# Optimization experiments

Hardware: AMD Instinct MI355X
Metric: run time of the kernel (lower is better)

## Reference

```python
import jax, jax.numpy as jnp
import numpy as np
from jax.ops import segment_sum

N_NODES = 50000
N_EDGES = 600000
HIDDEN = 128
N_FEAT = 128
N_CLASSES = 10
N_GRAPHS = 128


def setup_inputs() -> dict:
    key = jax.random.key(0)
    ks = jax.random.split(key, 16)
    x = jax.random.normal(ks[0], (N_NODES, N_FEAT), dtype=jnp.float32)
    edge_index = jax.random.randint(ks[1], (2, N_EDGES), 0, N_NODES, dtype=jnp.int64)
    batch = jnp.sort(jax.random.randint(ks[2], (N_NODES,), 0, N_GRAPHS, dtype=jnp.int64))
    def lin_init(k, fan_in, fan_out):
        s = 1.0 / np.sqrt(fan_in)
        return jax.random.uniform(k, (fan_in, fan_out), jnp.float32, -s, s)
    params = {
        'W1': lin_init(ks[3], N_FEAT, HIDDEN), 'b1': jnp.zeros((HIDDEN,), jnp.float32),
        'W2': lin_init(ks[4], HIDDEN, HIDDEN), 'b2': jnp.zeros((HIDDEN,), jnp.float32),
        'W3': lin_init(ks[5], HIDDEN, HIDDEN), 'b3': jnp.zeros((HIDDEN,), jnp.float32),
        'W4': lin_init(ks[6], HIDDEN, HIDDEN), 'b4': jnp.zeros((HIDDEN,), jnp.float32),
        'W5': lin_init(ks[7], HIDDEN, HIDDEN), 'b5': jnp.zeros((HIDDEN,), jnp.float32),
        'Wfc': lin_init(ks[8], HIDDEN, HIDDEN), 'bfc': jnp.zeros((HIDDEN,), jnp.float32),
        'Wlin': lin_init(ks[9], HIDDEN, N_CLASSES), 'blin': jnp.zeros((N_CLASSES,), jnp.float32),
    }
    return dict(x=x, edge_index=edge_index, batch=batch, **params)


def _gcn_edges(edge_index, n_nodes):
    # PyG GCNConv default: add self-loops, symmetric deg^-1/2 normalization.
    loop = jnp.arange(n_nodes, dtype=edge_index.dtype)
    row = jnp.concatenate([edge_index[0], loop])  # source (messages gathered from)
    col = jnp.concatenate([edge_index[1], loop])  # target (scatter-add into)
    deg = segment_sum(jnp.ones_like(col, dtype=jnp.float32), col, num_segments=n_nodes)
    dinv = jnp.where(deg > 0, jax.lax.rsqrt(deg), 0.0)
    norm = dinv[row] * dinv[col]  # [E+N]
    return row, col, norm


def _gcn_conv(x, W, b, row, col, norm, n_nodes):
    h = x @ W  # [N, out]
    agg = segment_sum(h[row] * norm[:, None], col, num_segments=n_nodes)
    return agg + b


def reference(x, edge_index, batch, W1, b1, W2, b2, W3, b3, W4, b4, W5, b5, Wfc, bfc, Wlin, blin):
    n = x.shape[0]
    row, col, norm = _gcn_edges(edge_index, n)
    h = jax.nn.relu(_gcn_conv(x, W1, b1, row, col, norm, n))
    h = jax.nn.relu(_gcn_conv(h, W2, b2, row, col, norm, n))
    h = jax.nn.relu(_gcn_conv(h, W3, b3, row, col, norm, n))
    h = jax.nn.relu(_gcn_conv(h, W4, b4, row, col, norm, n))
    h = jax.nn.relu(_gcn_conv(h, W5, b5, row, col, norm, n))
    h = jax.nn.relu(h @ Wfc + bfc)
    # global_mean_pool over batch ids
    sums = segment_sum(h, batch, num_segments=N_GRAPHS)
    cnts = segment_sum(jnp.ones((n,), h.dtype), batch, num_segments=N_GRAPHS)
    pooled = sums / jnp.maximum(cnts, 1.0)[:, None]  # [G, H]
    embeddings = pooled
    # dropout p=0.5 is identity in eval mode
    logits = pooled @ Wlin + blin  # [G, C]
    return logits, jnp.squeeze(embeddings)
```

## Files before the change

kernel.cpp:

```cpp
#include <hip/hip_runtime.h>

typedef __attribute__((ext_vector_type(8))) short short8;
typedef __attribute__((ext_vector_type(4))) float floatx4;
typedef __attribute__((ext_vector_type(4))) unsigned uintx4;
typedef __attribute__((ext_vector_type(8))) _Float16 half8;

static __device__ __forceinline__ unsigned short f2bf(float f) {
    unsigned u = __float_as_uint(f);
    u += 0x7fff + ((u >> 16) & 1);
    return (unsigned short)(u >> 16);
}
static __device__ __forceinline__ float bf2f(unsigned short h) {
    return __uint_as_float((unsigned)h << 16);
}
static __device__ __forceinline__ unsigned packsplit(float f) {
    unsigned short hi = f2bf(f);
    unsigned short lo = f2bf(f - bf2f(hi));
    return ((unsigned)hi << 16) | lo;
}


__global__ void count_kernel(const int* __restrict__ ei, int* degi, int E) {
    int e = blockIdx.x * 256 + threadIdx.x;
    if (e < E) atomicAdd(&degi[ei[E + e]], 1);
}

__global__ __launch_bounds__(256) void scan_bsum_kernel(const int* __restrict__ degi,
                                                        float* __restrict__ dinv,
                                                        int* bsum, int n) {
    int tid = threadIdx.x;
    int i = blockIdx.x * 256 + tid;
    int d = (i < n) ? degi[i] : 0;
    if (i < n) dinv[i] = rsqrtf((float)(d + 1));
    int v = d;
    #pragma unroll
    for (int off = 32; off > 0; off >>= 1) v += __shfl_down(v, off);
    __shared__ int ws[4];
    if ((tid & 63) == 0) ws[tid >> 6] = v;
    __syncthreads();
    if (tid == 0) bsum[blockIdx.x] = ws[0] + ws[1] + ws[2] + ws[3];
}

__global__ __launch_bounds__(256) void scan_emit_kernel(const int* __restrict__ degi,
                                                        const int* __restrict__ bsum,
                                                        int* rp, int* cursor, int n, int nb) {
    int tid = threadIdx.x;
    int bid = blockIdx.x;
    int contrib = 0;
    for (int t = tid; t < bid; t += 256) contrib += bsum[t];
    int cr = contrib;
    #pragma unroll
    for (int off = 32; off > 0; off >>= 1) cr += __shfl_down(cr, off);
    __shared__ int wr[4];
    __shared__ int s_boff;
    if ((tid & 63) == 0) wr[tid >> 6] = cr;
    __syncthreads();
    if (tid == 0) s_boff = wr[0] + wr[1] + wr[2] + wr[3];
    __syncthreads();

    int i = bid * 256 + tid;
    int v = (i < n) ? degi[i] : 0;
    int lane = tid & 63, wid = tid >> 6;
    int x = v;
    #pragma unroll
    for (int off = 1; off < 64; off <<= 1) {
        int y = __shfl_up(x, off);
        if (lane >= off) x += y;
    }
    __shared__ int ws[4];
    if (lane == 63) ws[wid] = x;
    __syncthreads();
    if (tid == 0) { int a = 0; for (int j = 0; j < 4; ++j) { int t = ws[j]; ws[j] = a; a += t; } }
    __syncthreads();
    int excl = x - v + ws[wid] + s_boff;
    if (i < n) { rp[i] = excl; cursor[i] = excl; }
    if (i == n - 1) rp[n] = excl + v;
}

__global__ void fill_kernel(const int* __restrict__ ei, const float* __restrict__ dinv,
                            int* cursor, long long* __restrict__ csr, int E) {
    int e = blockIdx.x * 256 + threadIdx.x;
    if (e >= E) return;
    int r = ei[e], c = ei[E + e];
    int pos = atomicAdd(&cursor[c], 1);
    float wv = dinv[r] * dinv[c];
    long long packed = (long long)(unsigned int)r
                     | ((long long)(unsigned int)__float_as_int(wv) << 32);
    csr[pos] = packed;
}


__global__ void packw_kernel(const float* w0, const float* w1, const float* w2,
                             const float* w3, const float* w4, const float* w5,
                             unsigned short* __restrict__ hi, unsigned short* __restrict__ lo) {
    int l = blockIdx.y;
    const float* W = (l == 0) ? w0 : (l == 1) ? w1 : (l == 2) ? w2
                   : (l == 3) ? w3 : (l == 4) ? w4 : w5;
    int idx = blockIdx.x * 256 + threadIdx.x;
    int k = idx >> 7, nn = idx & 127;
    float v = W[k * 128 + nn];
    unsigned short h = f2bf(v);
    unsigned short ls = f2bf(v - bf2f(h));
    hi[l * 16384 + nn * 128 + k] = h;
    lo[l * 16384 + nn * 128 + k] = ls;
}


#define WLDS_STRIDE 260

static __device__ __forceinline__ void stage_w(const unsigned short* __restrict__ Wth,
                                               const unsigned short* __restrict__ Wtl,
                                               unsigned short* Wlds, int tid) {
    #pragma unroll
    for (int it = 0; it < 8; ++it) {
        int c = it * 512 + tid;
        int row = c >> 5, piece = c & 31;
        const unsigned short* src = (piece < 16)
            ? (Wth + (size_t)row * 128 + piece * 8)
            : (Wtl + (size_t)row * 128 + (piece - 16) * 8);
        int dst = row * WLDS_STRIDE + ((piece < 16) ? piece * 8 : 128 + (piece - 16) * 8);
        *(short8*)&Wlds[dst] = *(const short8*)src;
    }
}

static __device__ __forceinline__ void unpack_u(uintx4 u0, uintx4 u1, short8& ah, short8& al) {
    #pragma unroll
    for (int j = 0; j < 4; ++j) {
        ah[j]     = (short)(u0[j] >> 16); al[j]     = (short)(u0[j] & 0xffff);
        ah[4 + j] = (short)(u1[j] >> 16); al[4 + j] = (short)(u1[j] & 0xffff);
    }
}

__global__ __launch_bounds__(512) void gemm_kernel(const unsigned* __restrict__ Ap,
                                                   const unsigned short* __restrict__ Wth,
                                                   const unsigned short* __restrict__ Wtl,
                                                   void* __restrict__ C, int n, int outf) {
    __shared__ unsigned short Wlds[128 * WLDS_STRIDE];
    int tid = threadIdx.x;
    int wave = tid >> 6, lane = tid & 63;
    int m = lane & 15, quad = lane >> 4;
    int row0 = blockIdx.x * 128 + wave * 16;
    int arow = row0 + m; if (arow > n - 1) arow = n - 1;
    size_t n16 = (size_t)n * 16;
    size_t n32 = (size_t)n * 32;
    const unsigned* abase = Ap + (size_t)arow * 16 + (quad & 1) * 8;
    int chalf = quad >> 1;

    uintx4 pa0[4], pa1[4];
    #pragma unroll
    for (int kc = 0; kc < 4; ++kc) {
        const unsigned* ap = abase + (size_t)(2 * kc + chalf) * n16;
        pa0[kc] = *(const uintx4*)ap;
        pa1[kc] = *(const uintx4*)(ap + 4);
    }

    stage_w(Wth, Wtl, Wlds, tid);

    floatx4 acc[8];
    #pragma unroll
    for (int ct = 0; ct < 8; ++ct) acc[ct] = (floatx4){0.f, 0.f, 0.f, 0.f};
    __syncthreads();

    #pragma unroll
    for (int kc = 0; kc < 4; ++kc) {
        short8 ah, al;
        unpack_u(pa0[kc], pa1[kc], ah, al);
        #pragma unroll
        for (int ct = 0; ct < 8; ++ct) {
            int base = (ct * 16 + m) * WLDS_STRIDE + kc * 32 + quad * 8;
            short8 wh = *(const short8*)&Wlds[base];
            short8 wl = *(const short8*)&Wlds[base + 128];
            acc[ct] = __builtin_amdgcn_mfma_f32_16x16x32_bf16(ah, wl, acc[ct], 0, 0, 0);
            acc[ct] = __builtin_amdgcn_mfma_f32_16x16x32_bf16(al, wh, acc[ct], 0, 0, 0);
            acc[ct] = __builtin_amdgcn_mfma_f32_16x16x32_bf16(ah, wh, acc[ct], 0, 0, 0);
        }
    }
    #pragma unroll
    for (int ct = 0; ct < 8; ++ct) {
        #pragma unroll
        for (int r = 0; r < 4; ++r) {
            int row = row0 + quad * 4 + r;
            if (row < n) {
                if (outf) {
                    ((float*)C)[(size_t)row * 128 + ct * 16 + m] = acc[ct][r];
                } else {
                    ((_Float16*)C)[(size_t)(ct >> 1) * n32 + (size_t)row * 32
                                   + (ct & 1) * 16 + m] = (_Float16)acc[ct][r];
                }
            }
        }
    }
}

__global__ __launch_bounds__(512) void gemm0_kernel(const float* __restrict__ X,
                                                    const unsigned short* __restrict__ Wth,
                                                    const unsigned short* __restrict__ Wtl,
                                                    _Float16* __restrict__ C, int n) {
    __shared__ unsigned short Wlds[128 * WLDS_STRIDE];
    int tid = threadIdx.x;
    int wave = tid >> 6, lane = tid & 63;
    int m = lane & 15, quad = lane >> 4;
    int row0 = blockIdx.x * 128 + wave * 16;
    int arow = row0 + m; if (arow > n - 1) arow = n - 1;
    size_t n32 = (size_t)n * 32;
    const float* aptr = X + (size_t)arow * 128 + quad * 8;

    floatx4 pf0[4], pf1[4];
    #pragma unroll
    for (int kc = 0; kc < 4; ++kc) {
        pf0[kc] = *(const floatx4*)(aptr + kc * 32);
        pf1[kc] = *(const floatx4*)(aptr + kc * 32 + 4);
    }

    stage_w(Wth, Wtl, Wlds, tid);

    floatx4 acc[8];
    #pragma unroll
    for (int ct = 0; ct < 8; ++ct) acc[ct] = (floatx4){0.f, 0.f, 0.f, 0.f};
    __syncthreads();

    #pragma unroll
    for (int kc = 0; kc < 4; ++kc) {
        short8 ah, al;
        #pragma unroll
        for (int j = 0; j < 8; ++j) {
            float fv = (j < 4) ? pf0[kc][j] : pf1[kc][j - 4];
            unsigned short h = f2bf(fv);
            ah[j] = (short)h;
            al[j] = (short)f2bf(fv - bf2f(h));
        }
        #pragma unroll
        for (int ct = 0; ct < 8; ++ct) {
            int base = (ct * 16 + m) * WLDS_STRIDE + kc * 32 + quad * 8;
            short8 wh = *(const short8*)&Wlds[base];
            short8 wl = *(const short8*)&Wlds[base + 128];
            acc[ct] = __builtin_amdgcn_mfma_f32_16x16x32_bf16(ah, wl, acc[ct], 0, 0, 0);
            acc[ct] = __builtin_amdgcn_mfma_f32_16x16x32_bf16(al, wh, acc[ct], 0, 0, 0);
            acc[ct] = __builtin_amdgcn_mfma_f32_16x16x32_bf16(ah, wh, acc[ct], 0, 0, 0);
        }
    }
    #pragma unroll
    for (int ct = 0; ct < 8; ++ct) {
        #pragma unroll
        for (int r = 0; r < 4; ++r) {
            int row = row0 + quad * 4 + r;
            if (row < n)
                C[(size_t)(ct >> 1) * n32 + (size_t)row * 32 + (ct & 1) * 16 + m] =
                    (_Float16)acc[ct][r];
        }
    }
}


__global__ __launch_bounds__(256) void agg_kernel(const _Float16* __restrict__ t,
                                                  const float* __restrict__ bias,
                                                  const int* __restrict__ rp,
                                                  const long long* __restrict__ csr,
                                                  const float* __restrict__ dinv,
                                                  unsigned* __restrict__ hp, int n, int nh) {
    int s = blockIdx.x & 7;
    int chunk = s & 3;
    int half = s >> 2;
    int nb = blockIdx.x >> 3;
    int group = threadIdx.x >> 2;
    int lane4 = threadIdx.x & 3;
    int j = half * nh + nb * 64 + group;
    int jend = half ? n : nh;
    if (j >= jend) return;
    size_t n32 = (size_t)n * 32;
    const _Float16* tc = t + (size_t)chunk * n32;
    int c8 = lane4 * 8;
    int p0 = rp[j], p1 = rp[j + 1];

    float dj = dinv[j];
    float wsf = dj * dj;
    half8 vs = *(const half8*)&tc[(size_t)j * 32 + c8];

    float acc[8];
    #pragma unroll
    for (int k = 0; k < 8; ++k) acc[k] = wsf * (float)vs[k];

    for (int p = p0; p < p1; p += 8) {
        int lim = p1 - 1;
        long long e[8];
        #pragma unroll
        for (int i = 0; i < 8; ++i) e[i] = csr[min(p + i, lim)];
        float w[8];
        #pragma unroll
        for (int i = 0; i < 8; ++i)
            w[i] = (p + i < p1) ? __int_as_float((int)(e[i] >> 32)) : 0.f;
        half8 v[8];
        #pragma unroll
        for (int i = 0; i < 8; ++i)
            v[i] = *(const half8*)&tc[(size_t)(int)e[i] * 32 + c8];
        #pragma unroll
        for (int i = 0; i < 8; ++i) {
            #pragma unroll
            for (int k = 0; k < 8; ++k) acc[k] += w[i] * (float)v[i][k];
        }
    }

    int cbase = chunk * 32 + c8;
    float4 b0 = *(const float4*)&bias[cbase];
    float4 b1 = *(const float4*)&bias[cbase + 4];
    float bb[8] = {b0.x, b0.y, b0.z, b0.w, b1.x, b1.y, b1.z, b1.w};
    unsigned st[8];
    #pragma unroll
    for (int k = 0; k < 8; ++k) st[k] = packsplit(fmaxf(acc[k] + bb[k], 0.f));

    size_t n16 = (size_t)n * 16;
    int hc = chunk * 2 + (lane4 >> 1);
    unsigned* dst = &hp[(size_t)hc * n16 + (size_t)j * 16 + (lane4 & 1) * 8];
    *(uint4*)dst = make_uint4(st[0], st[1], st[2], st[3]);
    *(uint4*)(dst + 4) = make_uint4(st[4], st[5], st[6], st[7]);
}


__global__ __launch_bounds__(256) void pool_kernel(const float* __restrict__ t,
                                                   const float* __restrict__ bfc,
                                                   const int* __restrict__ batch,
                                                   const float* __restrict__ Wlin,
                                                   const float* __restrict__ blin,
                                                   float* __restrict__ out, int n) {
    int g = blockIdx.x;
    int tid = threadIdx.x;
    int lo = 0, hi = n;
    while (lo < hi) { int m = (lo + hi) >> 1; if (batch[m] < g) lo = m + 1; else hi = m; }
    int start = lo;
    lo = start; hi = n;
    while (lo < hi) { int m = (lo + hi) >> 1; if (batch[m] < g + 1) lo = m + 1; else hi = m; }
    int end = lo;

    int lane = tid & 31, sub = tid >> 5;
    int c4 = lane * 4;
    float4 bv = *(const float4*)&bfc[c4];
    float sx = 0.f, sy = 0.f, sz = 0.f, sw = 0.f;
    for (int j = start + sub; j < end; j += 8) {
        float4 v = *(const float4*)&t[(size_t)j * 128 + c4];
        sx += fmaxf(v.x + bv.x, 0.f);
        sy += fmaxf(v.y + bv.y, 0.f);
        sz += fmaxf(v.z + bv.z, 0.f);
        sw += fmaxf(v.w + bv.w, 0.f);
    }
    __shared__ float red[8][128];
    red[sub][c4] = sx; red[sub][c4 + 1] = sy; red[sub][c4 + 2] = sz; red[sub][c4 + 3] = sw;
    __syncthreads();
    __shared__ float pooled[128];
    if (tid < 128) {
        float s = 0.f;
        #pragma unroll
        for (int k = 0; k < 8; ++k) s += red[k][tid];
        float pv = s / fmaxf((float)(end - start), 1.f);
        pooled[tid] = pv;
        out[1280 + g * 128 + tid] = pv;
    }
    __syncthreads();
    if (tid < 10) {
        float a = blin[tid];
        for (int k = 0; k < 128; ++k) a += pooled[k] * Wlin[k * 10 + tid];
        out[g * 10 + tid] = a;
    }
}


extern "C" void kernel_launch(void* const* d_in, const int* in_sizes, int n_in,
                              void* d_out, int out_size, void* d_ws, size_t ws_size,
                              hipStream_t stream) {
    const float* x     = (const float*)d_in[0];
    const int*   ei    = (const int*)d_in[1];
    const int*   batch = (const int*)d_in[2];
    const float* Wl[6] = {(const float*)d_in[3], (const float*)d_in[5], (const float*)d_in[7],
                          (const float*)d_in[9], (const float*)d_in[11], (const float*)d_in[13]};
    const float* bl[6] = {(const float*)d_in[4], (const float*)d_in[6], (const float*)d_in[8],
                          (const float*)d_in[10], (const float*)d_in[12], (const float*)d_in[14]};
    const float* Wlin = (const float*)d_in[15];
    const float* blin = (const float*)d_in[16];

    const int N = in_sizes[2];
    const int E = in_sizes[1] / 2;
    (void)n_in; (void)out_size; (void)ws_size;

    char* p = (char*)d_ws;
    auto carve = [&](size_t bytes) { void* r = (void*)p; p += (bytes + 255) & ~(size_t)255; return r; };
    void*           treg   = carve((size_t)N * 128 * 4);
    _Float16*       th     = (_Float16*)treg;
    float*          tf     = (float*)treg;
    unsigned*       hp     = (unsigned*)carve((size_t)N * 128 * 4);
    int*            degi   = (int*)carve((size_t)N * 4);
    float*          dinv   = (float*)carve((size_t)N * 4);
    int*            rp     = (int*)carve((size_t)(N + 1) * 4);
    int*            cursor = (int*)carve((size_t)N * 4);
    long long*      csr    = (long long*)carve((size_t)(E + N) * 8);
    int*            bsum   = (int*)carve(256 * 4);
    unsigned short* wth    = (unsigned short*)carve(6 * 16384 * 2);
    unsigned short* wtl    = (unsigned short*)carve(6 * 16384 * 2);

    int gN = (N + 255) / 256;
    hipMemsetAsync(degi, 0, (size_t)N * 4, stream);
    count_kernel<<<(E + 255) / 256, 256, 0, stream>>>(ei, degi, E);
    scan_bsum_kernel<<<gN, 256, 0, stream>>>(degi, dinv, bsum, N);
    scan_emit_kernel<<<gN, 256, 0, stream>>>(degi, bsum, rp, cursor, N, gN);
    fill_kernel<<<(E + 255) / 256, 256, 0, stream>>>(ei, dinv, cursor, csr, E);
    packw_kernel<<<dim3(64, 6), 256, 0, stream>>>(Wl[0], Wl[1], Wl[2], Wl[3], Wl[4], Wl[5],
                                                  wth, wtl);

    int NH = (N + 1) / 2;
    int gGemm = (N + 127) / 128;
    int gAgg  = 8 * ((NH + 63) / 64);
    gemm0_kernel<<<gGemm, 512, 0, stream>>>(x, wth, wtl, th, N);
    agg_kernel<<<gAgg, 256, 0, stream>>>(th, bl[0], rp, csr, dinv, hp, N, NH);
    for (int l = 1; l < 5; ++l) {
        gemm_kernel<<<gGemm, 512, 0, stream>>>(hp, wth + l * 16384, wtl + l * 16384,
                                               (void*)th, N, 0);
        agg_kernel<<<gAgg, 256, 0, stream>>>(th, bl[l], rp, csr, dinv, hp, N, NH);
    }
    gemm_kernel<<<gGemm, 512, 0, stream>>>(hp, wth + 5 * 16384, wtl + 5 * 16384,
                                           (void*)tf, N, 1);
    pool_kernel<<<128, 256, 0, stream>>>(tf, bl[5], batch, Wlin, blin, (float*)d_out, N);
}
```

Measured before the change: 413.7 us.

## Bucket nodes by degree for load-balanced aggregation; raise GEMM occupancy hint

Builds a degree histogram and a counting-sort order of nodes, so each aggregation wavefront handles nodes of similar in-degree instead of nodes in index order. The aim is to cut divergence and tail imbalance inside agg_kernel's edge loop. It also adds a min-blocks-per-CU hint to both GEMM kernels. The cost is three extra small preprocessing kernels and an indirect node lookup, and writes to the node-indexed output are no longer contiguous across neighbouring groups, which may hurt coalescing.

Measured after the change: 610.3 us. +47.5%, slower.

```diff
diff --git a/kernel.cpp b/kernel.cpp
--- a/kernel.cpp
+++ b/kernel.cpp
@@ -27,11 +27,17 @@
 
 __global__ __launch_bounds__(256) void scan_bsum_kernel(const int* __restrict__ degi,
                                                         float* __restrict__ dinv,
-                                                        int* bsum, int n) {
+                                                        int* bsum, int* hist, int n) {
+    __shared__ int sh[64];
     int tid = threadIdx.x;
+    if (tid < 64) sh[tid] = 0;
+    __syncthreads();
     int i = blockIdx.x * 256 + tid;
     int d = (i < n) ? degi[i] : 0;
-    if (i < n) dinv[i] = rsqrtf((float)(d + 1));
+    if (i < n) {
+        dinv[i] = rsqrtf((float)(d + 1));
+        atomicAdd(&sh[min(d, 63)], 1);
+    }
     int v = d;
     #pragma unroll
     for (int off = 32; off > 0; off >>= 1) v += __shfl_down(v, off);
@@ -39,6 +45,28 @@
     if ((tid & 63) == 0) ws[tid >> 6] = v;
     __syncthreads();
     if (tid == 0) bsum[blockIdx.x] = ws[0] + ws[1] + ws[2] + ws[3];
+    if (tid < 64 && sh[tid] > 0) atomicAdd(&hist[tid], sh[tid]);
+}
+
+__global__ void bucket_scan_kernel(const int* __restrict__ hist, int* hcur) {
+    int l = threadIdx.x;
+    int v = hist[l];
+    int x = v;
+    #pragma unroll
+    for (int off = 1; off < 64; off <<= 1) {
+        int y = __shfl_up(x, off);
+        if (l >= off) x += y;
+    }
+    hcur[l] = x - v;
+}
+
+__global__ void order_kernel(const int* __restrict__ degi, int* hcur,
+                             int* __restrict__ order, int n) {
+    int j = blockIdx.x * 256 + threadIdx.x;
+    if (j >= n) return;
+    int b = min(degi[j], 63);
+    int pos = atomicAdd(&hcur[b], 1);
+    order[pos] = j;
 }
 
 __global__ __launch_bounds__(256) void scan_emit_kernel(const int* __restrict__ degi,
@@ -131,10 +159,10 @@
     }
 }
 
-__global__ __launch_bounds__(512) void gemm_kernel(const unsigned* __restrict__ Ap,
-                                                   const unsigned short* __restrict__ Wth,
-                                                   const unsigned short* __restrict__ Wtl,
-                                                   void* __restrict__ C, int n, int outf) {
+__global__ __launch_bounds__(512, 4) void gemm_kernel(const unsigned* __restrict__ Ap,
+                                                      const unsigned short* __restrict__ Wth,
+                                                      const unsigned short* __restrict__ Wtl,
+                                                      void* __restrict__ C, int n, int outf) {
     __shared__ unsigned short Wlds[128 * WLDS_STRIDE];
     int tid = threadIdx.x;
     int wave = tid >> 6, lane = tid & 63;
@@ -192,10 +220,10 @@
     }
 }
 
-__global__ __launch_bounds__(512) void gemm0_kernel(const float* __restrict__ X,
-                                                    const unsigned short* __restrict__ Wth,
-                                                    const unsigned short* __restrict__ Wtl,
-                                                    _Float16* __restrict__ C, int n) {
+__global__ __launch_bounds__(512, 4) void gemm0_kernel(const float* __restrict__ X,
+                                                       const unsigned short* __restrict__ Wth,
+                                                       const unsigned short* __restrict__ Wtl,
+                                                       _Float16* __restrict__ C, int n) {
     __shared__ unsigned short Wlds[128 * WLDS_STRIDE];
     int tid = threadIdx.x;
     int wave = tid >> 6, lane = tid & 63;
@@ -257,6 +285,7 @@
                                                   const int* __restrict__ rp,
                                                   const long long* __restrict__ csr,
                                                   const float* __restrict__ dinv,
+                                                  const int* __restrict__ order,
                                                   unsigned* __restrict__ hp, int n, int nh) {
     int s = blockIdx.x & 7;
     int chunk = s & 3;
@@ -264,9 +293,10 @@
     int nb = blockIdx.x >> 3;
     int group = threadIdx.x >> 2;
     int lane4 = threadIdx.x & 3;
-    int j = half * nh + nb * 64 + group;
-    int jend = half ? n : nh;
-    if (j >= jend) return;
+    int idx = half * nh + nb * 64 + group;
+    int iend = half ? n : nh;
+    if (idx >= iend) return;
+    int j = order[idx];
     size_t n32 = (size_t)n * 32;
     const _Float16* tc = t + (size_t)chunk * n32;
     int c8 = lane4 * 8;
@@ -386,20 +416,26 @@
     _Float16*       th     = (_Float16*)treg;
     float*          tf     = (float*)treg;
     unsigned*       hp     = (unsigned*)carve((size_t)N * 128 * 4);
-    int*            degi   = (int*)carve((size_t)N * 4);
+    int*            degx   = (int*)carve((size_t)(N + 128) * 4);
+    int*            degi   = degx;
+    int*            hist   = degx + N;
+    int*            hcur   = degx + N + 64;
     float*          dinv   = (float*)carve((size_t)N * 4);
     int*            rp     = (int*)carve((size_t)(N + 1) * 4);
     int*            cursor = (int*)carve((size_t)N * 4);
+    int*            order  = (int*)carve((size_t)N * 4);
     long long*      csr    = (long long*)carve((size_t)(E + N) * 8);
     int*            bsum   = (int*)carve(256 * 4);
     unsigned short* wth    = (unsigned short*)carve(6 * 16384 * 2);
     unsigned short* wtl    = (unsigned short*)carve(6 * 16384 * 2);
 
     int gN = (N + 255) / 256;
-    hipMemsetAsync(degi, 0, (size_t)N * 4, stream);
+    hipMemsetAsync(degx, 0, (size_t)(N + 128) * 4, stream);
     count_kernel<<<(E + 255) / 256, 256, 0, stream>>>(ei, degi, E);
-    scan_bsum_kernel<<<gN, 256, 0, stream>>>(degi, dinv, bsum, N);
+    scan_bsum_kernel<<<gN, 256, 0, stream>>>(degi, dinv, bsum, hist, N);
+    bucket_scan_kernel<<<1, 64, 0, stream>>>(hist, hcur);
     scan_emit_kernel<<<gN, 256, 0, stream>>>(degi, bsum, rp, cursor, N, gN);
+    order_kernel<<<gN, 256, 0, stream>>>(degi, hcur, order, N);
     fill_kernel<<<(E + 255) / 256, 256, 0, stream>>>(ei, dinv, cursor, csr, E);
     packw_kernel<<<dim3(64, 6), 256, 0, stream>>>(Wl[0], Wl[1], Wl[2], Wl[3], Wl[4], Wl[5],
                                                   wth, wtl);
@@ -408,11 +444,11 @@
     int gGemm = (N + 127) / 128;
     int gAgg  = 8 * ((NH + 63) / 64);
     gemm0_kernel<<<gGemm, 512, 0, stream>>>(x, wth, wtl, th, N);
-    agg_kernel<<<gAgg, 256, 0, stream>>>(th, bl[0], rp, csr, dinv, hp, N, NH);
+    agg_kernel<<<gAgg, 256, 0, stream>>>(th, bl[0], rp, csr, dinv, order, hp, N, NH);
     for (int l = 1; l < 5; ++l) {
         gemm_kernel<<<gGemm, 512, 0, stream>>>(hp, wth + l * 16384, wtl + l * 16384,
                                                (void*)th, N, 0);
-        agg_kernel<<<gAgg, 256, 0, stream>>>(th, bl[l], rp, csr, dinv, hp, N, NH);
+        agg_kernel<<<gAgg, 256, 0, stream>>>(th, bl[l], rp, csr, dinv, order, hp, N, NH);
     }
     gemm_kernel<<<gGemm, 512, 0, stream>>>(hp, wth + 5 * 16384, wtl + 5 * 16384,
                                            (void*)tf, N, 1);
```

## Factor GCN normalization into GEMM epilogue and shrink CSR to 4-byte indices

Applied to the files above, without the earlier changes.

Splits the symmetric norm dinv[r]*dinv[c]: the GEMM epilogues scale each output row by dinv of the source row, and the aggregation multiplies the summed neighbours by dinv of the target at the end. This lets the CSR store only 4-byte source indices, halving edge-list traffic, and removes the per-edge weight multiply. The aggregation loop is split into an unmasked main loop plus a masked tail. Launch bounds gain an occupancy hint of 4. A side effect is that the outf GEMM path never applies dinv, so the fp32 final layer stays unscaled as it should. Rounding changes slightly because pre-scaled values are stored in fp16.

After: 402.6 us. 1.03x faster.

```diff
diff --git a/kernel.cpp b/kernel.cpp
--- a/kernel.cpp
+++ b/kernel.cpp
@@ -77,16 +77,13 @@
     if (i == n - 1) rp[n] = excl + v;
 }
 
-__global__ void fill_kernel(const int* __restrict__ ei, const float* __restrict__ dinv,
-                            int* cursor, long long* __restrict__ csr, int E) {
+__global__ void fill_kernel(const int* __restrict__ ei, int* cursor,
+                            int* __restrict__ csr, int E) {
     int e = blockIdx.x * 256 + threadIdx.x;
     if (e >= E) return;
     int r = ei[e], c = ei[E + e];
     int pos = atomicAdd(&cursor[c], 1);
-    float wv = dinv[r] * dinv[c];
-    long long packed = (long long)(unsigned int)r
-                     | ((long long)(unsigned int)__float_as_int(wv) << 32);
-    csr[pos] = packed;
+    csr[pos] = r;
 }
 
 
@@ -131,10 +128,11 @@
     }
 }
 
-__global__ __launch_bounds__(512) void gemm_kernel(const unsigned* __restrict__ Ap,
-                                                   const unsigned short* __restrict__ Wth,
-                                                   const unsigned short* __restrict__ Wtl,
-                                                   void* __restrict__ C, int n, int outf) {
+__global__ __launch_bounds__(512, 4) void gemm_kernel(const unsigned* __restrict__ Ap,
+                                                      const unsigned short* __restrict__ Wth,
+                                                      const unsigned short* __restrict__ Wtl,
+                                                      const float* __restrict__ dinv,
+                                                      void* __restrict__ C, int n, int outf) {
     __shared__ unsigned short Wlds[128 * WLDS_STRIDE];
     int tid = threadIdx.x;
     int wave = tid >> 6, lane = tid & 63;
@@ -175,6 +173,11 @@
             acc[ct] = __builtin_amdgcn_mfma_f32_16x16x32_bf16(ah, wh, acc[ct], 0, 0, 0);
         }
     }
+
+    float dv[4];
+    #pragma unroll
+    for (int r = 0; r < 4; ++r) dv[r] = dinv[min(row0 + quad * 4 + r, n - 1)];
+
     #pragma unroll
     for (int ct = 0; ct < 8; ++ct) {
         #pragma unroll
@@ -185,17 +188,18 @@
                     ((float*)C)[(size_t)row * 128 + ct * 16 + m] = acc[ct][r];
                 } else {
                     ((_Float16*)C)[(size_t)(ct >> 1) * n32 + (size_t)row * 32
-                                   + (ct & 1) * 16 + m] = (_Float16)acc[ct][r];
+                                   + (ct & 1) * 16 + m] = (_Float16)(acc[ct][r] * dv[r]);
                 }
             }
         }
     }
 }
 
-__global__ __launch_bounds__(512) void gemm0_kernel(const float* __restrict__ X,
-                                                    const unsigned short* __restrict__ Wth,
-                                                    const unsigned short* __restrict__ Wtl,
-                                                    _Float16* __restrict__ C, int n) {
+__global__ __launch_bounds__(512, 4) void gemm0_kernel(const float* __restrict__ X,
+                                                       const unsigned short* __restrict__ Wth,
+                                                       const unsigned short* __restrict__ Wtl,
+                                                       const float* __restrict__ dinv,
+                                                       _Float16* __restrict__ C, int n) {
     __shared__ unsigned short Wlds[128 * WLDS_STRIDE];
     int tid = threadIdx.x;
     int wave = tid >> 6, lane = tid & 63;
@@ -239,6 +243,11 @@
             acc[ct] = __builtin_amdgcn_mfma_f32_16x16x32_bf16(ah, wh, acc[ct], 0, 0, 0);
         }
     }
+
+    float dv[4];
+    #pragma unroll
+    for (int r = 0; r < 4; ++r) dv[r] = dinv[min(row0 + quad * 4 + r, n - 1)];
+
     #pragma unroll
     for (int ct = 0; ct < 8; ++ct) {
         #pragma unroll
@@ -246,7 +255,7 @@
             int row = row0 + quad * 4 + r;
             if (row < n)
                 C[(size_t)(ct >> 1) * n32 + (size_t)row * 32 + (ct & 1) * 16 + m] =
-                    (_Float16)acc[ct][r];
+                    (_Float16)(acc[ct][r] * dv[r]);
         }
     }
 }
@@ -255,7 +264,7 @@
 __global__ __launch_bounds__(256) void agg_kernel(const _Float16* __restrict__ t,
                                                   const float* __restrict__ bias,
                                                   const int* __restrict__ rp,
-                                                  const long long* __restrict__ csr,
+                                                  const int* __restrict__ csr,
                                                   const float* __restrict__ dinv,
                                                   unsigned* __restrict__ hp, int n, int nh) {
     int s = blockIdx.x & 7;
@@ -273,30 +282,43 @@
     int p0 = rp[j], p1 = rp[j + 1];
 
     float dj = dinv[j];
-    float wsf = dj * dj;
     half8 vs = *(const half8*)&tc[(size_t)j * 32 + c8];
 
     float acc[8];
     #pragma unroll
-    for (int k = 0; k < 8; ++k) acc[k] = wsf * (float)vs[k];
-
-    for (int p = p0; p < p1; p += 8) {
-        int lim = p1 - 1;
-        long long e[8];
-        #pragma unroll
-        for (int i = 0; i < 8; ++i) e[i] = csr[min(p + i, lim)];
-        float w[8];
+    for (int k = 0; k < 8; ++k) acc[k] = (float)vs[k];
+
+    int p = p0;
+    for (; p + 8 <= p1; p += 8) {
+        int e[8];
+        #pragma unroll
+        for (int i = 0; i < 8; ++i) e[i] = csr[p + i];
+        half8 v[8];
         #pragma unroll
         for (int i = 0; i < 8; ++i)
-            w[i] = (p + i < p1) ? __int_as_float((int)(e[i] >> 32)) : 0.f;
-        half8 v[8];
-        #pragma unroll
-        for (int i = 0; i < 8; ++i)
-            v[i] = *(const half8*)&tc[(size_t)(int)e[i] * 32 + c8];
+            v[i] = *(const half8*)&tc[(size_t)e[i] * 32 + c8];
         #pragma unroll
         for (int i = 0; i < 8; ++i) {
             #pragma unroll
-            for (int k = 0; k < 8; ++k) acc[k] += w[i] * (float)v[i][k];
+            for (int k = 0; k < 8; ++k) acc[k] += (float)v[i][k];
+        }
+    }
+    if (p < p1) {
+        int lim = p1 - 1;
+        int e[8];
+        #pragma unroll
+        for (int i = 0; i < 8; ++i) e[i] = csr[min(p + i, lim)];
+        float msk[8];
+        #pragma unroll
+        for (int i = 0; i < 8; ++i) msk[i] = (p + i < p1) ? 1.f : 0.f;
+        half8 v[8];
+        #pragma unroll
+        for (int i = 0; i < 8; ++i)
+            v[i] = *(const half8*)&tc[(size_t)e[i] * 32 + c8];
+        #pragma unroll
+        for (int i = 0; i < 8; ++i) {
+            #pragma unroll
+            for (int k = 0; k < 8; ++k) acc[k] += msk[i] * (float)v[i][k];
         }
     }
 
@@ -306,7 +328,7 @@
     float bb[8] = {b0.x, b0.y, b0.z, b0.w, b1.x, b1.y, b1.z, b1.w};
     unsigned st[8];
     #pragma unroll
-    for (int k = 0; k < 8; ++k) st[k] = packsplit(fmaxf(acc[k] + bb[k], 0.f));
+    for (int k = 0; k < 8; ++k) st[k] = packsplit(fmaxf(fmaf(dj, acc[k], bb[k]), 0.f));
 
     size_t n16 = (size_t)n * 16;
     int hc = chunk * 2 + (lane4 >> 1);
@@ -390,7 +412,7 @@
     float*          dinv   = (float*)carve((size_t)N * 4);
     int*            rp     = (int*)carve((size_t)(N + 1) * 4);
     int*            cursor = (int*)carve((size_t)N * 4);
-    long long*      csr    = (long long*)carve((size_t)(E + N) * 8);
+    int*            csr    = (int*)carve((size_t)E * 4);
     int*            bsum   = (int*)carve(256 * 4);
     unsigned short* wth    = (unsigned short*)carve(6 * 16384 * 2);
     unsigned short* wtl    = (unsigned short*)carve(6 * 16384 * 2);
@@ -400,21 +422,21 @@
     count_kernel<<<(E + 255) / 256, 256, 0, stream>>>(ei, degi, E);
     scan_bsum_kernel<<<gN, 256, 0, stream>>>(degi, dinv, bsum, N);
     scan_emit_kernel<<<gN, 256, 0, stream>>>(degi, bsum, rp, cursor, N, gN);
-    fill_kernel<<<(E + 255) / 256, 256, 0, stream>>>(ei, dinv, cursor, csr, E);
+    fill_kernel<<<(E + 255) / 256, 256, 0, stream>>>(ei, cursor, csr, E);
     packw_kernel<<<dim3(64, 6), 256, 0, stream>>>(Wl[0], Wl[1], Wl[2], Wl[3], Wl[4], Wl[5],
                                                   wth, wtl);
 
     int NH = (N + 1) / 2;
     int gGemm = (N + 127) / 128;
     int gAgg  = 8 * ((NH + 63) / 64);
-    gemm0_kernel<<<gGemm, 512, 0, stream>>>(x, wth, wtl, th, N);
+    gemm0_kernel<<<gGemm, 512, 0, stream>>>(x, wth, wtl, dinv, th, N);
     agg_kernel<<<gAgg, 256, 0, stream>>>(th, bl[0], rp, csr, dinv, hp, N, NH);
     for (int l = 1; l < 5; ++l) {
         gemm_kernel<<<gGemm, 512, 0, stream>>>(hp, wth + l * 16384, wtl + l * 16384,
-                                               (void*)th, N, 0);
+                                               dinv, (void*)th, N, 0);
         agg_kernel<<<gAgg, 256, 0, stream>>>(th, bl[l], rp, csr, dinv, hp, N, NH);
     }
     gemm_kernel<<<gGemm, 512, 0, stream>>>(hp, wth + 5 * 16384, wtl + 5 * 16384,
-                                           (void*)tf, N, 1);
+                                           dinv, (void*)tf, N, 1);
     pool_kernel<<<128, 256, 0, stream>>>(tf, bl[5], batch, Wlin, blin, (float*)d_out, N);
 }
```
